# Performance work log

Hardware: AMD Instinct MI355X
Metric: run time of the kernel (lower is better)

Reference implementation:

```python
import jax, jax.numpy as jnp
import numpy as np

D_MODEL = 1024
N_HEADS = 16
D_HEAD = 64
B, S = 2, 2048


def setup_inputs() -> dict:
    key = jax.random.key(0)
    ks = jax.random.split(key, 16)
    HDH = N_HEADS * D_HEAD
    s = 0.02
    return {
        "h": jax.random.normal(ks[0], (B, S, D_MODEL), dtype=jnp.float32),
        "att_mask": jax.random.randint(ks[1], (B, S), 0, 2) > 0,
        "Wq": jax.random.normal(ks[2], (D_MODEL, HDH), dtype=jnp.float32) * s,
        "bq": jnp.zeros((HDH,), dtype=jnp.float32),
        "Wkv": jax.random.normal(ks[3], (D_MODEL, 2 * HDH), dtype=jnp.float32) * s,
        "bkv": jnp.zeros((2 * HDH,), dtype=jnp.float32),
        "Wo": jax.random.normal(ks[4], (HDH, D_MODEL), dtype=jnp.float32) * s,
        "bo": jnp.zeros((D_MODEL,), dtype=jnp.float32),
        "W1": jax.random.normal(ks[5], (D_MODEL, D_MODEL), dtype=jnp.float32) * s,
        "b1": jnp.zeros((D_MODEL,), dtype=jnp.float32),
        "W2": jax.random.normal(ks[6], (D_MODEL, D_MODEL), dtype=jnp.float32) * s,
        "b2": jnp.zeros((D_MODEL,), dtype=jnp.float32),
        "ln_g": jnp.ones((D_MODEL,), dtype=jnp.float32),
        "ln_b": jnp.zeros((D_MODEL,), dtype=jnp.float32),
    }


def _layer_norm(x, g, b, eps=1e-6):
    mu = jnp.mean(x, axis=-1, keepdims=True)
    var = jnp.mean(jnp.square(x - mu), axis=-1, keepdims=True)
    return (x - mu) * jax.lax.rsqrt(var + eps) * g + b


def reference(h, att_mask, Wq, bq, Wkv, bkv, Wo, bo, W1, b1, W2, b2, ln_g, ln_b):
    bz, ln, _ = h.shape
    scale = 1.0 / (D_HEAD ** 0.5)
    q = (h @ Wq + bq).reshape(bz, ln, N_HEADS, D_HEAD)
    kv = h @ Wkv + bkv
    k, v = jnp.split(kv, 2, axis=-1)
    k = k.reshape(bz, ln, N_HEADS, D_HEAD)
    v = v.reshape(bz, ln, N_HEADS, D_HEAD)
    # scores: [b, heads, len_q, len_k]
    scores = jnp.einsum('bqhd,bkhd->bhqk', q, k) * scale
    scores = jnp.where(att_mask[:, None, None, :], -1e9, scores)
    probs = jax.nn.softmax(scores, axis=-1)
    att = jnp.einsum('bhqk,bkhd->bqhd', probs, v).reshape(bz, ln, N_HEADS * D_HEAD)
    att_out = att @ Wo + bo
    # glu_type == 1
    g = jax.nn.sigmoid(h @ W1 + b1) * (h @ W2 + b2)
    return _layer_norm(h + att_out + g, ln_g, ln_b)
```

## Files before the change

kernel.cpp:

```cpp
#include <hip/hip_runtime.h>
#include <hip/hip_bf16.h>


typedef short bf16x8 __attribute__((ext_vector_type(8)));
typedef float f32x4  __attribute__((ext_vector_type(4)));
typedef float f32x16 __attribute__((ext_vector_type(16)));
typedef unsigned int u32x4 __attribute__((ext_vector_type(4)));

typedef const __attribute__((address_space(1))) void* gas_cvp;
typedef __attribute__((address_space(3))) void* las_vp;

__device__ __forceinline__ void gload_lds16(const void* g, void* l) {
  __builtin_amdgcn_global_load_lds((gas_cvp)g, (las_vp)l, 16, 0, 0);
}

__device__ __forceinline__ short f2bf(float f) {
  __hip_bfloat16 h = __float2bfloat16(f);
  return *reinterpret_cast<short*>(&h);
}
__device__ __forceinline__ float bf2f(short s) {
  unsigned u = ((unsigned)(unsigned short)s) << 16;
  return __builtin_bit_cast(float, u);
}

#if __has_builtin(__builtin_amdgcn_exp2f)
#define EXP2(x) __builtin_amdgcn_exp2f(x)
#else
#define EXP2(x) exp2f(x)
#endif

constexpr int BATCH = 2;
constexpr int SEQ   = 2048;
constexpr int NH    = 16;
constexpr int MROWS = BATCH * SEQ;
constexpr int NSPLIT = 2;
constexpr int KSPL   = SEQ / NSPLIT;
constexpr int RH     = MROWS * NH;


__global__ __launch_bounds__(256) void cvt_bf16(const float* __restrict__ src,
                                                short* __restrict__ dst, int n4) {
  int i = blockIdx.x * 256 + threadIdx.x;
  if (i >= n4) return;
  float4 v = reinterpret_cast<const float4*>(src)[i];
  short4 o;
  o.x = f2bf(v.x); o.y = f2bf(v.y); o.z = f2bf(v.z); o.w = f2bf(v.w);
  reinterpret_cast<short4*>(dst)[i] = o;
}

struct WtA {
  const float* s[6];
  short* d[6];
  int st[6];
  int mul[6];
  int add[6];
};
__global__ __launch_bounds__(256) void wtrans6(WtA a) {
  __shared__ float tile[32][33];
  const float* __restrict__ src = a.s[blockIdx.z];
  short* __restrict__ dst = a.d[blockIdx.z];
  const int stride = a.st[blockIdx.z];
  const int mul = a.mul[blockIdx.z], add = a.add[blockIdx.z];
  const int tx = threadIdx.x & 31, ty = threadIdx.x >> 5;
  const int n0 = blockIdx.x * 32, k0 = blockIdx.y * 32;
  #pragma unroll
  for (int i = 0; i < 32; i += 8)
    tile[ty + i][tx] = src[(size_t)(k0 + ty + i) * stride + n0 + tx];
  __syncthreads();
  #pragma unroll
  for (int i = 0; i < 32; i += 8)
    dst[(size_t)((n0 + ty + i) * mul + add) * 1024 + k0 + tx] = f2bf(tile[tx][ty + i]);
}

__global__ __launch_bounds__(256) void vtrans(const short* __restrict__ qkv,
                                              short* __restrict__ vt) {
  __shared__ short tile[32][33];
  const int tx = threadIdx.x & 31, ty = threadIdx.x >> 5;
  const int s0 = blockIdx.x * 32, d0 = blockIdx.y * 32, b = blockIdx.z;
  #pragma unroll
  for (int i = 0; i < 32; i += 8)
    tile[ty + i][tx] = qkv[(size_t)(b * SEQ + s0 + ty + i) * 3072 + 2048 + d0 + tx];
  __syncthreads();
  #pragma unroll
  for (int i = 0; i < 32; i += 8)
    vt[(size_t)(b * 1024 + d0 + ty + i) * SEQ + s0 + tx] = tile[tx][ty + i];
}

__global__ void pack_bias(const float* __restrict__ bq, const float* __restrict__ bkv,
                          const float* __restrict__ b1, const float* __restrict__ b2,
                          float* __restrict__ ball) {
  int i = blockIdx.x * 256 + threadIdx.x;
  if (i < 1024) ball[i] = bq[i];
  else if (i < 3072) ball[i] = bkv[i - 1024];
  else if (i < 4096) {
    const int j = i - 3072;
    ball[3072 + 2 * j] = b1[j];
    ball[3072 + 2 * j + 1] = b2[j];
  }
}

__device__ __forceinline__ bool mask_at(const void* mp, int idx, int flag) {
  if (flag == 1) return ((const int*)mp)[idx] != 0;
  if (flag == 2) return ((const float*)mp)[idx] != 0.f;
  return ((const unsigned char*)mp)[idx] != 0;
}

__global__ __launch_bounds__(256) void premask(const void* __restrict__ msk,
                                               float* __restrict__ mbL) {
  __shared__ int si, sf;
  const unsigned* m = (const unsigned*)msk;
  if (threadIdx.x == 0) { si = 1; sf = 1; }
  __syncthreads();
  bool oki = true, okf = true;
  for (int i = threadIdx.x; i < 1024; i += 256) {
    unsigned v = m[i];
    oki = oki && (v <= 1u);
    okf = okf && (v == 0u || v == 0x3F800000u);
  }
  if (!oki) si = 0;
  if (!okf) sf = 0;
  __syncthreads();
  const int flag = si ? 1 : (sf ? 2 : 0);
  int i = blockIdx.x * 256 + threadIdx.x;
  if (i < MROWS) mbL[i] = mask_at(msk, i, flag) ? -1.442695e9f : -8.0f;
}


template <int BN>
__global__ __launch_bounds__(256) void gemm_bf16(const short* __restrict__ A,
                                                 const short* __restrict__ BT,
                                                 const float* __restrict__ bias,
                                                 short* __restrict__ outp, int N) {
  constexpr int NF = BN / 64;
  __shared__ short Alds[128 * 64];
  __shared__ short Blds[BN * 64];
  const int tid = threadIdx.x;
  const int w = tid >> 6, l = tid & 63, lr = l & 15;
  const int wr = w >> 1, wc = w & 1;
  const int bm = blockIdx.y, bn = blockIdx.x;

  f32x4 acc[4][2 * NF] = {};

  const int srow = tid >> 3;
  const int schunk = (tid & 7) ^ (srow & 7);
  const short* Ab = A  + (size_t)(bm * 128 + srow) * 1024 + schunk * 8;
  const short* Bb = BT + (size_t)(bn * BN + srow) * 1024 + schunk * 8;

  const int cg = (l >> 4) ^ (l & 3), fl = (l >> 2) & 1;
  const short* ard[2] = { &Alds[(wr * 64 + lr) * 64 + cg * 8 + fl * 32],
                          &Alds[(wr * 64 + lr) * 64 + cg * 8 + 32 - fl * 32] };
  const short* brd[2] = { &Blds[(wc * (BN / 2) + lr) * 64 + cg * 8 + fl * 32],
                          &Blds[(wc * (BN / 2) + lr) * 64 + cg * 8 + 32 - fl * 32] };

  for (int kt = 0; kt < 16; ++kt) {
    const int kb = kt * 64;
    __syncthreads();
    #pragma unroll
    for (int q = 0; q < 4; ++q)
      gload_lds16(Ab + (size_t)q * 32 * 1024 + kb, &Alds[q * 2048 + tid * 8]);
    #pragma unroll
    for (int q = 0; q < BN / 32; ++q)
      gload_lds16(Bb + (size_t)q * 32 * 1024 + kb, &Blds[q * 2048 + tid * 8]);
    asm volatile("s_waitcnt vmcnt(0)" ::: "memory");
    __syncthreads();

    #pragma unroll
    for (int s = 0; s < 2; ++s) {
      bf16x8 af[4], bfr[2 * NF];
      #pragma unroll
      for (int m = 0; m < 4; ++m)
        af[m] = *reinterpret_cast<const bf16x8*>(ard[s] + m * 16 * 64);
      #pragma unroll
      for (int n = 0; n < 2 * NF; ++n)
        bfr[n] = *reinterpret_cast<const bf16x8*>(brd[s] + n * 16 * 64);
      #pragma unroll
      for (int m = 0; m < 4; ++m)
        #pragma unroll
        for (int n = 0; n < 2 * NF; ++n)
          acc[m][n] = __builtin_amdgcn_mfma_f32_16x16x32_bf16(af[m], bfr[n], acc[m][n], 0, 0, 0);
    }
  }

  const int g = l >> 4;
  #pragma unroll
  for (int m = 0; m < 4; ++m) {
    const int row = bm * 128 + wr * 64 + m * 16 + g * 4;
    #pragma unroll
    for (int n = 0; n < 2 * NF; ++n) {
      const int col = bn * BN + wc * (BN / 2) + n * 16 + lr;
      const float bv = bias[col];
      #pragma unroll
      for (int r = 0; r < 4; ++r)
        outp[(size_t)(row + r) * N + col] = f2bf(acc[m][n][r] + bv);
    }
  }
}

__global__ __launch_bounds__(256) void gemm_qkvglu(const short* __restrict__ A,
                                                   const short* __restrict__ BT,
                                                   const float* __restrict__ bias,
                                                   short* __restrict__ qkv,
                                                   short* __restrict__ x1) {
  __shared__ short Alds[128 * 64];
  __shared__ short Blds[128 * 64];
  const int tid = threadIdx.x;
  const int w = tid >> 6, l = tid & 63, lr = l & 15;
  const int wr = w >> 1, wc = w & 1;
  const int bm = blockIdx.y, bn = blockIdx.x;

  f32x4 acc[4][4] = {};

  const int srow = tid >> 3;
  const int schunk = (tid & 7) ^ (srow & 7);
  const short* Ab = A  + (size_t)(bm * 128 + srow) * 1024 + schunk * 8;
  const short* Bb = BT + (size_t)(bn * 128 + srow) * 1024 + schunk * 8;

  const int cg = (l >> 4) ^ (l & 3), fl = (l >> 2) & 1;
  const short* ard[2] = { &Alds[(wr * 64 + lr) * 64 + cg * 8 + fl * 32],
                          &Alds[(wr * 64 + lr) * 64 + cg * 8 + 32 - fl * 32] };
  const short* brd[2] = { &Blds[(wc * 64 + lr) * 64 + cg * 8 + fl * 32],
                          &Blds[(wc * 64 + lr) * 64 + cg * 8 + 32 - fl * 32] };

  for (int kt = 0; kt < 16; ++kt) {
    const int kb = kt * 64;
    __syncthreads();
    #pragma unroll
    for (int q = 0; q < 4; ++q) {
      gload_lds16(Ab + (size_t)q * 32 * 1024 + kb, &Alds[q * 2048 + tid * 8]);
      gload_lds16(Bb + (size_t)q * 32 * 1024 + kb, &Blds[q * 2048 + tid * 8]);
    }
    asm volatile("s_waitcnt vmcnt(0)" ::: "memory");
    __syncthreads();

    #pragma unroll
    for (int s = 0; s < 2; ++s) {
      bf16x8 af[4], bfr[4];
      #pragma unroll
      for (int m = 0; m < 4; ++m)
        af[m] = *reinterpret_cast<const bf16x8*>(ard[s] + m * 16 * 64);
      #pragma unroll
      for (int n = 0; n < 4; ++n)
        bfr[n] = *reinterpret_cast<const bf16x8*>(brd[s] + n * 16 * 64);
      #pragma unroll
      for (int m = 0; m < 4; ++m)
        #pragma unroll
        for (int n = 0; n < 4; ++n)
          acc[m][n] = __builtin_amdgcn_mfma_f32_16x16x32_bf16(af[m], bfr[n], acc[m][n], 0, 0, 0);
    }
  }

  const int g = l >> 4;
  const bool isGlu = (bn >= 24);
  #pragma unroll
  for (int m = 0; m < 4; ++m) {
    const int row = bm * 128 + wr * 64 + m * 16 + g * 4;
    #pragma unroll
    for (int n = 0; n < 4; ++n) {
      const int col = bn * 128 + wc * 64 + n * 16 + lr;
      const float bv = bias[col];
      #pragma unroll
      for (int r = 0; r < 4; ++r) {
        const float v = acc[m][n][r] + bv;
        if (!isGlu) {
          qkv[(size_t)(row + r) * 3072 + col] = f2bf(v);
        } else {
          const float vp = __shfl_xor(v, 1);
          if (!(lr & 1)) {
            const int col2 = col - 3072;
            x1[(size_t)(row + r) * 1024 + (col2 >> 1)] = f2bf(vp / (1.f + __expf(-v)));
          }
        }
      }
    }
  }
}

constexpr int KB = 64;
constexpr int KSLOT = 8 * 66;
constexpr int VSLOT = 8 * 66;

__global__ __launch_bounds__(256) void attn_kernel(const short* __restrict__ qkv,
                                                   const short* __restrict__ vt,
                                                   const float* __restrict__ mbL,
                                                   short* __restrict__ opart,
                                                   float* __restrict__ spart) {
  __shared__ short Kl[2][KSLOT * 8];
  __shared__ short Vl[2][VSLOT * 8];
  __shared__ float mb[KSPL];

  const int tid = threadIdx.x;
  const int w = tid >> 6, lane = tid & 63, ql = lane & 31, hi = lane >> 5;
  const int sp = blockIdx.x & (NSPLIT - 1), qb = blockIdx.x / NSPLIT;
  const int h = blockIdx.y, b = blockIdx.z;
  const int qrow = qb * 128 + w * 32 + ql;
  const int kofs = sp * KSPL;

  bf16x8 qf[4];
  {
    const short* qp = qkv + (size_t)(b * SEQ + qrow) * 3072 + h * 64;
    #pragma unroll
    for (int c = 0; c < 4; ++c)
      qf[c] = *reinterpret_cast<const bf16x8*>(qp + c * 16 + hi * 8);
  }

  const short* gkbase = qkv + (size_t)(b * SEQ + kofs) * 3072 + 1024 + h * 64
                        + (size_t)(tid >> 3) * 3072 + (tid & 7) * 8;
  const short* gvbase = vt + ((size_t)(b * 1024 + h * 64) + (tid >> 3)) * SEQ + kofs
                        + (tid & 7) * 8;
  short* kwr = &Kl[0][((tid & 7) * 66 + (tid >> 3)) * 8];
  short* vwr = &Vl[0][((tid & 7) * 66 + (tid >> 3)) * 8];

  u32x4 kreg0, kreg1, vreg0, vreg1;
  auto loadTile = [&](int kt) {
    const short* gk = gkbase + (size_t)kt * KB * 3072;
    kreg0 = *reinterpret_cast<const u32x4*>(gk);
    kreg1 = *reinterpret_cast<const u32x4*>(gk + 32 * 3072);
    const short* gv = gvbase + kt * KB;
    vreg0 = *reinterpret_cast<const u32x4*>(gv);
    vreg1 = *reinterpret_cast<const u32x4*>(gv + 32 * SEQ);
  };
  auto writeTile = [&](int buf) {
    short* kd = kwr + buf * KSLOT * 8;
    *reinterpret_cast<u32x4*>(kd)          = kreg0;
    *reinterpret_cast<u32x4*>(kd + 32 * 8) = kreg1;
    short* vd = vwr + buf * VSLOT * 8;
    *reinterpret_cast<u32x4*>(vd)          = vreg0;
    *reinterpret_cast<u32x4*>(vd + 32 * 8) = vreg1;
  };

  float s_run = 0.f;
  f32x16 oacc0 = {}, oacc1 = {};

  gload_lds16(mbL + b * SEQ + kofs + tid * 4, &mb[tid * 4]);
  loadTile(0);
  writeTile(0);
  __syncthreads();

  const short* krd = &Kl[0][(hi * 66 + ql) * 8];
  const short* vrd = &Vl[0][(hi * 66 + ql) * 8];

  constexpr int NT = KSPL / KB;
  for (int kt = 0; kt < NT; ++kt) {
    const int cur = kt & 1;
    if (kt + 1 < NT) loadTile(kt + 1);
    const short* Kb = krd + cur * KSLOT * 8;
    const short* Vb = vrd + cur * VSLOT * 8;

    #pragma unroll
    for (int t2 = 0; t2 < 2; ++t2) {
      f32x16 sc = {};
      __builtin_amdgcn_s_setprio(1);
      #pragma unroll
      for (int c = 0; c < 4; ++c) {
        bf16x8 kf = *reinterpret_cast<const bf16x8*>(Kb + (c * 132 + t2 * 32) * 8);
        sc = __builtin_amdgcn_mfma_f32_32x32x16_bf16(kf, qf[c], sc, 0, 0, 0);
      }
      __builtin_amdgcn_s_setprio(0);
      float p[16];
      #pragma unroll
      for (int u = 0; u < 4; ++u) {
        float4 m4 = *reinterpret_cast<const float4*>(&mb[kt * KB + t2 * 32 + u * 8 + hi * 4]);
        p[4 * u + 0] = EXP2(fmaf(sc[4 * u + 0], 0.18033688f, m4.x));
        p[4 * u + 1] = EXP2(fmaf(sc[4 * u + 1], 0.18033688f, m4.y));
        p[4 * u + 2] = EXP2(fmaf(sc[4 * u + 2], 0.18033688f, m4.z));
        p[4 * u + 3] = EXP2(fmaf(sc[4 * u + 3], 0.18033688f, m4.w));
      }
      {
        float a0 = (p[0] + p[1]) + (p[2] + p[3]);
        float a1 = (p[4] + p[5]) + (p[6] + p[7]);
        float a2 = (p[8] + p[9]) + (p[10] + p[11]);
        float a3 = (p[12] + p[13]) + (p[14] + p[15]);
        s_run += (a0 + a1) + (a2 + a3);
      }
      unsigned P[8];
      #pragma unroll
      for (int j = 0; j < 8; ++j)
        asm("v_cvt_pk_bf16_f32 %0, %1, %2" : "=v"(P[j]) : "v"(p[2 * j]), "v"(p[2 * j + 1]));
      asm("v_permlane32_swap_b32 %0, %1" : "+v"(P[0]), "+v"(P[2]));
      asm("v_permlane32_swap_b32 %0, %1" : "+v"(P[1]), "+v"(P[3]));
      asm("v_permlane32_swap_b32 %0, %1" : "+v"(P[4]), "+v"(P[6]));
      asm("v_permlane32_swap_b32 %0, %1" : "+v"(P[5]), "+v"(P[7]));
      u32x4 c0 = { P[0], P[1], P[2], P[3] };
      u32x4 c1 = { P[4], P[5], P[6], P[7] };
      bf16x8 pf[2] = { __builtin_bit_cast(bf16x8, c0), __builtin_bit_cast(bf16x8, c1) };

      __builtin_amdgcn_s_setprio(1);
      #pragma unroll
      for (int ch = 0; ch < 2; ++ch) {
        const int gb = (t2 * 4 + ch * 2) * 66;
        bf16x8 v0 = *reinterpret_cast<const bf16x8*>(Vb + gb * 8);
        bf16x8 v1 = *reinterpret_cast<const bf16x8*>(Vb + (gb + 32) * 8);
        oacc0 = __builtin_amdgcn_mfma_f32_32x32x16_bf16(v0, pf[ch], oacc0, 0, 0, 0);
        oacc1 = __builtin_amdgcn_mfma_f32_32x32x16_bf16(v1, pf[ch], oacc1, 0, 0, 0);
      }
      __builtin_amdgcn_s_setprio(0);
    }

    if (kt + 1 < NT) {
      writeTile(cur ^ 1);
      __syncthreads();
    }
  }

  const float sT = s_run + __shfl_xor(s_run, 32);
  const size_t obase = (size_t)sp * RH * 64 + (size_t)(b * SEQ + qrow) * 1024 + h * 64;
  #pragma unroll
  for (int dt = 0; dt < 2; ++dt) {
    #pragma unroll
    for (int u = 0; u < 4; ++u) {
      short4 st;
      const f32x16& oa = dt ? oacc1 : oacc0;
      st.x = f2bf(oa[4 * u + 0]);
      st.y = f2bf(oa[4 * u + 1]);
      st.z = f2bf(oa[4 * u + 2]);
      st.w = f2bf(oa[4 * u + 3]);
      *reinterpret_cast<short4*>(&opart[obase + dt * 32 + u * 8 + hi * 4]) = st;
    }
  }
  if (hi == 0)
    spart[sp * RH + (b * SEQ + qrow) * NH + h] = sT;
}

__global__ __launch_bounds__(256) void attn_merge(const short* __restrict__ opart,
                                                  const float* __restrict__ spart,
                                                  short* __restrict__ att) {
  const int idx = blockIdx.x * 256 + threadIdx.x;
  const int rh = idx >> 3;
  const size_t base = (size_t)rh * 64 + (idx & 7) * 8;
  float acc[8] = {};
  float ss = 0.f;
  #pragma unroll
  for (int s = 0; s < NSPLIT; ++s) {
    bf16x8 o = *reinterpret_cast<const bf16x8*>(&opart[(size_t)s * RH * 64 + base]);
    #pragma unroll
    for (int j = 0; j < 8; ++j) acc[j] += bf2f(o[j]);
    ss += spart[s * RH + rh];
  }
  const float inv = 1.f / ss;
  bf16x8 r;
  #pragma unroll
  for (int j = 0; j < 8; ++j) r[j] = f2bf(acc[j] * inv);
  *reinterpret_cast<bf16x8*>(&att[base]) = r;
}

__global__ __launch_bounds__(256) void ln_kernel(const float* __restrict__ h,
                                                 const short* __restrict__ ao,
                                                 const short* __restrict__ gl,
                                                 const float* __restrict__ gamma,
                                                 const float* __restrict__ beta,
                                                 float* __restrict__ out) {
  const int row = blockIdx.x;
  const size_t base = (size_t)row * 1024;
  const int t = threadIdx.x;
  __shared__ float red[4];
  float x[4];
  #pragma unroll
  for (int j = 0; j < 4; ++j) {
    const int c = t + j * 256;
    x[j] = h[base + c] + bf2f(ao[base + c]) + bf2f(gl[base + c]);
  }
  float s = x[0] + x[1] + x[2] + x[3];
  #pragma unroll
  for (int d = 1; d < 64; d <<= 1) s += __shfl_xor(s, d);
  if ((t & 63) == 0) red[t >> 6] = s;
  __syncthreads();
  const float mu = (red[0] + red[1] + red[2] + red[3]) * (1.f / 1024.f);
  __syncthreads();
  float vs = 0.f;
  #pragma unroll
  for (int j = 0; j < 4; ++j) { const float dx = x[j] - mu; vs += dx * dx; }
  #pragma unroll
  for (int d = 1; d < 64; d <<= 1) vs += __shfl_xor(vs, d);
  if ((t & 63) == 0) red[t >> 6] = vs;
  __syncthreads();
  const float var = (red[0] + red[1] + red[2] + red[3]) * (1.f / 1024.f);
  const float rs = rsqrtf(var + 1e-6f);
  #pragma unroll
  for (int j = 0; j < 4; ++j) {
    const int c = t + j * 256;
    out[base + c] = (x[j] - mu) * rs * gamma[c] + beta[c];
  }
}


extern "C" void kernel_launch(void* const* d_in, const int* in_sizes, int n_in,
                              void* d_out, int out_size, void* d_ws, size_t ws_size,
                              hipStream_t stream) {
  const float* h   = (const float*)d_in[0];
  const void*  msk = d_in[1];
  const float* Wq  = (const float*)d_in[2];
  const float* bq  = (const float*)d_in[3];
  const float* Wkv = (const float*)d_in[4];
  const float* bkv = (const float*)d_in[5];
  const float* Wo  = (const float*)d_in[6];
  const float* bo  = (const float*)d_in[7];
  const float* W1  = (const float*)d_in[8];
  const float* b1  = (const float*)d_in[9];
  const float* W2  = (const float*)d_in[10];
  const float* b2  = (const float*)d_in[11];
  const float* lng = (const float*)d_in[12];
  const float* lnb = (const float*)d_in[13];
  float* out = (float*)d_out;

  char* ws = (char*)d_ws;
  size_t off = 0;
  auto alloc = [&](size_t bytes) {
    char* p = ws + off;
    off += (bytes + 255) & ~(size_t)255;
    return p;
  };
  short* X     = (short*)alloc((size_t)MROWS * 1024 * 2);
  short* WALL  = (short*)alloc((size_t)5120 * 1024 * 2);
  short* WoT   = (short*)alloc((size_t)1024 * 1024 * 2);
  float* ball  = (float*)alloc(5120 * 4);
  float* MBL   = (float*)alloc((size_t)MROWS * 4);
  short* QKV   = (short*)alloc((size_t)MROWS * 3072 * 2);
  short* VT    = (short*)alloc((size_t)BATCH * 1024 * SEQ * 2);
  short* ATT   = (short*)alloc((size_t)MROWS * 1024 * 2);
  short* X1    = (short*)alloc((size_t)MROWS * 1024 * 2);
  short* AO    = (short*)alloc((size_t)MROWS * 1024 * 2);
  short* OP    = (short*)alloc((size_t)NSPLIT * RH * 64 * 2);
  float* SP    = (float*)alloc((size_t)NSPLIT * RH * 4);
  if (off > ws_size) return;

  cvt_bf16<<<4096, 256, 0, stream>>>(h, X, MROWS * 1024 / 4);
  WtA wa;
  wa.s[0] = Wq;          wa.d[0] = WALL;                wa.st[0] = 1024;  wa.mul[0] = 1; wa.add[0] = 0;
  wa.s[1] = Wkv;         wa.d[1] = WALL + 1024 * 1024;  wa.st[1] = 2048;  wa.mul[1] = 1; wa.add[1] = 0;
  wa.s[2] = Wkv + 1024;  wa.d[2] = WALL + 2048 * 1024;  wa.st[2] = 2048;  wa.mul[2] = 1; wa.add[2] = 0;
  wa.s[3] = Wo;          wa.d[3] = WoT;                 wa.st[3] = 1024;  wa.mul[3] = 1; wa.add[3] = 0;
  wa.s[4] = W1;          wa.d[4] = WALL + 3072 * 1024;  wa.st[4] = 1024;  wa.mul[4] = 2; wa.add[4] = 0;
  wa.s[5] = W2;          wa.d[5] = WALL + 3072 * 1024;  wa.st[5] = 1024;  wa.mul[5] = 2; wa.add[5] = 1;
  wtrans6<<<dim3(32, 32, 6), 256, 0, stream>>>(wa);
  pack_bias<<<16, 256, 0, stream>>>(bq, bkv, b1, b2, ball);
  premask<<<16, 256, 0, stream>>>(msk, MBL);

  gemm_qkvglu<<<dim3(40, 32), 256, 0, stream>>>(X, WALL, ball, QKV, X1);
  vtrans<<<dim3(64, 32, 2), 256, 0, stream>>>(QKV, VT);
  attn_kernel<<<dim3(16 * NSPLIT, 16, 2), 256, 0, stream>>>(QKV, VT, MBL, OP, SP);
  attn_merge<<<RH * 8 / 256, 256, 0, stream>>>(OP, SP, ATT);
  gemm_bf16<64><<<dim3(16, 32), 256, 0, stream>>>(ATT, WoT, bo, AO, 1024);
  ln_kernel<<<MROWS, 256, 0, stream>>>(h, AO, X1, lng, lnb, out);
}
```

Before: 173.2 us.

## Rewrite fused QKV/GLU GEMM with 128x256 tiles and triple-buffered async LDS pipeline

The fused QKV+GLU projection GEMM now uses 512-thread blocks computing 128x256 tiles, with a 3-stage dynamic-LDS ring. Global-to-LDS loads for k-step t+2 are issued in half-k chunks while MFMAs run on step t, and partial vmcnt waits replace the full drain-and-sync of each iteration. It also adds a grouped block-index swizzle for L2 reuse and raises wave priority around the MFMA burst. The cost is 144 KB of LDS per block, which allows only one block per CU, and more intricate wait-count bookkeeping.

```diff
diff --git a/kernel.cpp b/kernel.cpp
--- a/kernel.cpp
+++ b/kernel.cpp
@@ -125,7 +125,6 @@
   if (i < MROWS) mbL[i] = mask_at(msk, i, flag) ? -1.442695e9f : -8.0f;
 }
 
-
 template <int BN>
 __global__ __launch_bounds__(256) void gemm_bf16(const short* __restrict__ A,
                                                  const short* __restrict__ BT,
@@ -196,67 +195,86 @@
   }
 }
 
-__global__ __launch_bounds__(256) void gemm_qkvglu(const short* __restrict__ A,
-                                                   const short* __restrict__ BT,
-                                                   const float* __restrict__ bias,
-                                                   short* __restrict__ qkv,
-                                                   short* __restrict__ x1) {
-  __shared__ short Alds[128 * 64];
-  __shared__ short Blds[128 * 64];
+__global__ __launch_bounds__(512) void gemm_qkvglu8(const short* __restrict__ A,
+                                                    const short* __restrict__ BT,
+                                                    const float* __restrict__ bias,
+                                                    short* __restrict__ qkv,
+                                                    short* __restrict__ x1) {
+  extern __shared__ short lds[];
   const int tid = threadIdx.x;
-  const int w = tid >> 6, l = tid & 63, lr = l & 15;
-  const int wr = w >> 1, wc = w & 1;
-  const int bm = blockIdx.y, bn = blockIdx.x;
+  const int w = tid >> 6, l = tid & 63, lr = l & 15, g = l >> 4;
+  const int wr = w >> 2, wc = w & 3;
+  const int idx = blockIdx.x;
+  const int swz = (idx & 7) * 80 + (idx >> 3);
+  const int bn = swz / 32, bm = swz % 32;
+
+  const int arow = tid >> 2, ac2 = tid & 3;
+  const int lc8 = (ac2 ^ ((arow >> 1) & 3)) * 8;
+  const short* aSrc = A + (size_t)(bm * 128 + arow) * 1024 + lc8;
+  const short* bSrc = BT + (size_t)(bn * 256 + arow) * 1024 + lc8;
+  short* aDst = lds + tid * 8;
+  short* bDst = lds + 8192 + tid * 8;
+
+  auto stageKhalf = [&](int t, int s) {
+    const int buf = (t % 3) * 24576;
+    const int kof = t * 64 + s * 32;
+    gload_lds16(aSrc + kof, aDst + buf + s * 4096);
+    gload_lds16(bSrc + kof, bDst + buf + s * 8192);
+    gload_lds16(bSrc + (size_t)128 * 1024 + kof, bDst + buf + s * 8192 + 4096);
+  };
+
+  const int cg8 = (g ^ ((lr >> 1) & 3)) * 8;
+  const short* aRd = lds + (wr * 64 + lr) * 32 + cg8;
+  const short* bRd = lds + 8192 + (wc * 64 + lr) * 32 + cg8;
 
   f32x4 acc[4][4] = {};
 
-  const int srow = tid >> 3;
-  const int schunk = (tid & 7) ^ (srow & 7);
-  const short* Ab = A  + (size_t)(bm * 128 + srow) * 1024 + schunk * 8;
-  const short* Bb = BT + (size_t)(bn * 128 + srow) * 1024 + schunk * 8;
-
-  const int cg = (l >> 4) ^ (l & 3), fl = (l >> 2) & 1;
-  const short* ard[2] = { &Alds[(wr * 64 + lr) * 64 + cg * 8 + fl * 32],
-                          &Alds[(wr * 64 + lr) * 64 + cg * 8 + 32 - fl * 32] };
-  const short* brd[2] = { &Blds[(wc * 64 + lr) * 64 + cg * 8 + fl * 32],
-                          &Blds[(wc * 64 + lr) * 64 + cg * 8 + 32 - fl * 32] };
-
-  for (int kt = 0; kt < 16; ++kt) {
-    const int kb = kt * 64;
-    __syncthreads();
-    #pragma unroll
-    for (int q = 0; q < 4; ++q) {
-      gload_lds16(Ab + (size_t)q * 32 * 1024 + kb, &Alds[q * 2048 + tid * 8]);
-      gload_lds16(Bb + (size_t)q * 32 * 1024 + kb, &Blds[q * 2048 + tid * 8]);
-    }
-    asm volatile("s_waitcnt vmcnt(0)" ::: "memory");
-    __syncthreads();
-
+  stageKhalf(0, 0); stageKhalf(0, 1); stageKhalf(1, 0); stageKhalf(1, 1);
+  asm volatile("s_waitcnt vmcnt(9)" ::: "memory");
+  __syncthreads();
+
+  for (int t = 0; t < 16; ++t) {
+    const int buf = (t % 3) * 24576;
     #pragma unroll
     for (int s = 0; s < 2; ++s) {
-      bf16x8 af[4], bfr[4];
+      if (t + 2 < 16) stageKhalf(t + 2, s);
+      bf16x8 af[4], bfv[4];
       #pragma unroll
       for (int m = 0; m < 4; ++m)
-        af[m] = *reinterpret_cast<const bf16x8*>(ard[s] + m * 16 * 64);
+        af[m] = *reinterpret_cast<const bf16x8*>(aRd + buf + s * 4096 + m * 512);
       #pragma unroll
       for (int n = 0; n < 4; ++n)
-        bfr[n] = *reinterpret_cast<const bf16x8*>(brd[s] + n * 16 * 64);
+        bfv[n] = *reinterpret_cast<const bf16x8*>(bRd + buf + s * 8192 + n * 512);
+      __builtin_amdgcn_s_setprio(1);
       #pragma unroll
       for (int m = 0; m < 4; ++m)
         #pragma unroll
         for (int n = 0; n < 4; ++n)
-          acc[m][n] = __builtin_amdgcn_mfma_f32_16x16x32_bf16(af[m], bfr[n], acc[m][n], 0, 0, 0);
-    }
-  }
-
-  const int g = l >> 4;
-  const bool isGlu = (bn >= 24);
+          acc[m][n] = __builtin_amdgcn_mfma_f32_16x16x32_bf16(af[m], bfv[n], acc[m][n], 0, 0, 0);
+      __builtin_amdgcn_s_setprio(0);
+      if (t <= 13) {
+        asm volatile("s_waitcnt vmcnt(9)" ::: "memory");
+        __syncthreads();
+      } else if (t == 14) {
+        if (s == 0) asm volatile("s_waitcnt vmcnt(6)" ::: "memory");
+        else        asm volatile("s_waitcnt vmcnt(3)" ::: "memory");
+        __syncthreads();
+      } else {
+        if (s == 0) {
+          asm volatile("s_waitcnt vmcnt(0)" ::: "memory");
+          __syncthreads();
+        }
+      }
+    }
+  }
+
+  const bool isGlu = (bn >= 12);
   #pragma unroll
   for (int m = 0; m < 4; ++m) {
     const int row = bm * 128 + wr * 64 + m * 16 + g * 4;
     #pragma unroll
     for (int n = 0; n < 4; ++n) {
-      const int col = bn * 128 + wc * 64 + n * 16 + lr;
+      const int col = bn * 256 + wc * 64 + n * 16 + lr;
       const float bv = bias[col];
       #pragma unroll
       for (int r = 0; r < 4; ++r) {
@@ -265,10 +283,9 @@
           qkv[(size_t)(row + r) * 3072 + col] = f2bf(v);
         } else {
           const float vp = __shfl_xor(v, 1);
-          if (!(lr & 1)) {
-            const int col2 = col - 3072;
-            x1[(size_t)(row + r) * 1024 + (col2 >> 1)] = f2bf(vp / (1.f + __expf(-v)));
-          }
+          if (!(lr & 1))
+            x1[(size_t)(row + r) * 1024 + ((col - 3072) >> 1)] =
+                f2bf(vp / (1.f + __expf(-v)));
         }
       }
     }
@@ -523,6 +540,9 @@
   float* SP    = (float*)alloc((size_t)NSPLIT * RH * 4);
   if (off > ws_size) return;
 
+  hipFuncSetAttribute(reinterpret_cast<const void*>(gemm_qkvglu8),
+                      hipFuncAttributeMaxDynamicSharedMemorySize, 3 * 24576 * 2);
+
   cvt_bf16<<<4096, 256, 0, stream>>>(h, X, MROWS * 1024 / 4);
   WtA wa;
   wa.s[0] = Wq;          wa.d[0] = WALL;                wa.st[0] = 1024;  wa.mul[0] = 1; wa.add[0] = 0;
@@ -535,7 +555,7 @@
   pack_bias<<<16, 256, 0, stream>>>(bq, bkv, b1, b2, ball);
   premask<<<16, 256, 0, stream>>>(msk, MBL);
 
-  gemm_qkvglu<<<dim3(40, 32), 256, 0, stream>>>(X, WALL, ball, QKV, X1);
+  gemm_qkvglu8<<<640, 512, 3 * 24576 * 2, stream>>>(X, WALL, ball, QKV, X1);
   vtrans<<<dim3(64, 32, 2), 256, 0, stream>>>(QKV, VT);
   attn_kernel<<<dim3(16 * NSPLIT, 16, 2), 256, 0, stream>>>(QKV, VT, MBL, OP, SP);
   attn_merge<<<RH * 8 / 256, 256, 0, stream>>>(OP, SP, ATT);
```

New measurement: 199.2 us. 1.15x slower.
